# Optimization experiments

Measured on AMD Instinct MI355X. Metric: run time of the kernel, lower is better.

## Reference

```python
import jax, jax.numpy as jnp
import numpy as np

NUM_HEADS = 32
NUM_KV_HEADS = 8
HEAD_DIM = 128
ROPE_THETA = 10000.0


def rotate_half(x):
    x1, x2 = jnp.split(x, 2, axis=-1)
    return jnp.concatenate((-x2, x1), axis=-1)


def setup_inputs() -> dict:
    key = jax.random.key(0)
    ks = jax.random.split(key, 5)
    B, S, H = 1, 2048, 4096
    KV = NUM_KV_HEADS * HEAD_DIM
    return {
        "hidden_states": jax.random.normal(ks[0], (B, S, H), dtype=jnp.float32),
        "position_ids": jnp.arange(S, dtype=jnp.int64 if jax.config.jax_enable_x64 else jnp.int32)[None, :].repeat(B, axis=0),
        "Wq": jax.random.normal(ks[1], (H, H), dtype=jnp.float32) * 0.02,
        "Wk": jax.random.normal(ks[2], (KV, H), dtype=jnp.float32) * 0.02,
        "Wv": jax.random.normal(ks[3], (KV, H), dtype=jnp.float32) * 0.02,
        "Wo": jax.random.normal(ks[4], (H, H), dtype=jnp.float32) * 0.02,
    }


def reference(hidden_states, position_ids, Wq, Wk, Wv, Wo):
    B, S, H = hidden_states.shape
    nh, nkv, hd = NUM_HEADS, NUM_KV_HEADS, HEAD_DIM
    n_rep = nh // nkv

    # QKV projections (torch Linear: y = x @ W^T)
    q = jnp.einsum('bsh,oh->bso', hidden_states, Wq).reshape(B, S, nh, hd).transpose(0, 2, 1, 3)
    k = jnp.einsum('bsh,oh->bso', hidden_states, Wk).reshape(B, S, nkv, hd).transpose(0, 2, 1, 3)
    v = jnp.einsum('bsh,oh->bso', hidden_states, Wv).reshape(B, S, nkv, hd).transpose(0, 2, 1, 3)

    # RoPE: cos/sin [B, 1, S, hd]
    inv_freq = 1.0 / (ROPE_THETA ** (jnp.arange(0, hd, 2, dtype=jnp.float32) / hd))
    freqs = position_ids.astype(jnp.float32)[..., None] * inv_freq  # [B, S, hd/2]
    emb = jnp.concatenate((freqs, freqs), axis=-1)                  # [B, S, hd]
    cos = jnp.cos(emb)[:, None, :, :]
    sin = jnp.sin(emb)[:, None, :, :]
    q = q * cos + rotate_half(q) * sin
    k = k * cos + rotate_half(k) * sin

    # GQA repeat_kv: [B, nkv, S, hd] -> [B, nh, S, hd]
    k = jnp.repeat(k, n_rep, axis=1)
    v = jnp.repeat(v, n_rep, axis=1)

    # eager attention with causal mask, softmax in fp32
    scores = jnp.einsum('bhqd,bhkd->bhqk', q, k) / jnp.sqrt(jnp.float32(hd))
    causal = jnp.tril(jnp.ones((S, S), dtype=bool))
    scores = jnp.where(causal[None, None], scores, jnp.finfo(scores.dtype).min)
    probs = jax.nn.softmax(scores.astype(jnp.float32), axis=-1).astype(q.dtype)
    attn = jnp.einsum('bhqk,bhkd->bhqd', probs, v)

    out = attn.transpose(0, 2, 1, 3).reshape(B, S, nh * hd)
    return jnp.einsum('bso,ho->bsh', out, Wo)
```

## Files before the change

kernel.cpp:

```cpp
#include <hip/hip_runtime.h>

typedef __bf16 bf16x8 __attribute__((ext_vector_type(8)));
typedef float f32x4 __attribute__((ext_vector_type(4)));
typedef unsigned int u32x4 __attribute__((ext_vector_type(4)));
typedef unsigned short u16x4 __attribute__((ext_vector_type(4)));

#define S_LEN 2048
#define HDIM  4096
#define KVDIM 1024
#define NHEAD 32
#define NKV   8
#define QKVN  6144

__device__ __forceinline__ unsigned short f2b(float x) {
    unsigned int u = __builtin_bit_cast(unsigned int, x);
    u = (u + 0x7FFFu + ((u >> 16) & 1u)) >> 16;
    return (unsigned short)u;
}
__device__ __forceinline__ float b2f(unsigned short b) {
    unsigned int u = ((unsigned int)b) << 16;
    return __builtin_bit_cast(float, u);
}

__device__ __forceinline__ void gl_lds16(const void* g, void* s) {
    __builtin_amdgcn_global_load_lds(
        (const __attribute__((address_space(1))) unsigned int*)g,
        (__attribute__((address_space(3))) unsigned int*)s, 16, 0, 0);
}

__global__ void cvt_all(const float* __restrict__ hid, const float* __restrict__ Wq,
                        const float* __restrict__ Wk, const float* __restrict__ Wv,
                        unsigned short* __restrict__ hb, unsigned short* __restrict__ Wqkvb) {
    const int NH = S_LEN * HDIM / 4;
    const int NQ = HDIM * HDIM / 4;
    const int NK = KVDIM * HDIM / 4;
    int i = blockIdx.x * 256 + threadIdx.x;
    const float* src;
    unsigned short* dst;
    int off;
    if (i < NH) { src = hid; dst = hb; off = i; }
    else if (i < NH + NQ) { src = Wq; dst = Wqkvb; off = i - NH; }
    else if (i < NH + NQ + NK) { src = Wk; dst = Wqkvb + (size_t)HDIM * HDIM; off = i - NH - NQ; }
    else { src = Wv; dst = Wqkvb + (size_t)(HDIM + KVDIM) * HDIM; off = i - NH - NQ - NK; }
    f32x4 v = ((const f32x4*)src)[off];
    u16x4 o;
    o.x = f2b(v.x); o.y = f2b(v.y); o.z = f2b(v.z); o.w = f2b(v.w);
    ((u16x4*)dst)[off] = o;
}

__global__ void cvt_kernel(const float* __restrict__ in, unsigned short* __restrict__ out, int n4) {
    int i = blockIdx.x * 256 + threadIdx.x;
    if (i >= n4) return;
    f32x4 v = ((const f32x4*)in)[i];
    u16x4 o;
    o.x = f2b(v.x); o.y = f2b(v.y); o.z = f2b(v.z); o.w = f2b(v.w);
    ((u16x4*)out)[i] = o;
}

template <int MODE>
__device__ __forceinline__ void gemm_body(const unsigned short* __restrict__ A,
                                          const unsigned short* __restrict__ B,
                                          void* __restrict__ Cv,
                                          int M, int N, int K, int m0, int n0, int cn0,
                                          unsigned short (*As)[64], unsigned short (*Bs)[64]) {
    const int tid = threadIdx.x;
    const int w = tid >> 6, lane = tid & 63, quad = lane >> 4, l15 = lane & 15;
    const int wy = w >> 1, wx = w & 1;
    const int srowb = w * 32 + (lane >> 3);
    const int gchunk = (lane & 7) ^ (lane >> 3);
    const int lcol = (lane & 7) * 8;

    f32x4 acc[4][4] = {};

    for (int k0 = 0; k0 < K; k0 += 64) {
#pragma unroll
        for (int p = 0; p < 4; ++p) {
            int r = srowb + p * 8;
            gl_lds16(&A[(size_t)(m0 + r) * K + k0 + gchunk * 8], &As[r][lcol]);
            gl_lds16(&B[(size_t)(n0 + r) * K + k0 + gchunk * 8], &Bs[r][lcol]);
        }
        __syncthreads();
#pragma unroll
        for (int t = 0; t < 2; ++t) {
            bf16x8 af[4], bfr[4];
#pragma unroll
            for (int mb = 0; mb < 4; ++mb)
                af[mb] = *(const bf16x8*)&As[wy * 64 + mb * 16 + l15][(((t * 4 + quad) ^ (l15 & 7)) * 8)];
#pragma unroll
            for (int nb = 0; nb < 4; ++nb)
                bfr[nb] = *(const bf16x8*)&Bs[wx * 64 + nb * 16 + l15][(((t * 4 + quad) ^ (l15 & 7)) * 8)];
#pragma unroll
            for (int mb = 0; mb < 4; ++mb)
#pragma unroll
                for (int nb = 0; nb < 4; ++nb)
                    acc[mb][nb] = __builtin_amdgcn_mfma_f32_16x16x32_bf16(af[mb], bfr[nb], acc[mb][nb], 0, 0, 0);
        }
        __syncthreads();
    }
#pragma unroll
    for (int mb = 0; mb < 4; ++mb)
#pragma unroll
        for (int nb = 0; nb < 4; ++nb)
#pragma unroll
            for (int r = 0; r < 4; ++r) {
                int row = m0 + wy * 64 + mb * 16 + quad * 4 + r;
                int col = cn0 + wx * 64 + nb * 16 + l15;
                float v = acc[mb][nb][r];
                if (MODE == 0)
                    ((unsigned short*)Cv)[(size_t)row * N + col] = f2b(v);
                else if (MODE == 1)
                    ((unsigned short*)Cv)[(size_t)col * M + row] = f2b(v);
                else
                    ((float*)Cv)[(size_t)row * N + col] = v;
            }
}

template <int MODE>
__global__ __launch_bounds__(256) void gemm_nt(const unsigned short* __restrict__ A,
                                               const unsigned short* __restrict__ B,
                                               void* __restrict__ Cv, int M, int N, int K) {
    __shared__ unsigned short As[128][64];
    __shared__ unsigned short Bs[128][64];
    gemm_body<MODE>(A, B, Cv, M, N, K, blockIdx.y * 128, blockIdx.x * 128, blockIdx.x * 128, As, Bs);
}

__global__ __launch_bounds__(256) void gemm_qkv(const unsigned short* __restrict__ A,
                                                const unsigned short* __restrict__ W,
                                                unsigned short* __restrict__ Q,
                                                unsigned short* __restrict__ Kc,
                                                unsigned short* __restrict__ Vt,
                                                int M, int K) {
    __shared__ unsigned short As[128][64];
    __shared__ unsigned short Bs[128][64];
    const int bx = blockIdx.x, m0 = blockIdx.y * 128, n0 = bx * 128;
    if (bx < 32)
        gemm_body<0>(A, W, Q, M, HDIM, K, m0, n0, n0, As, Bs);
    else if (bx < 40)
        gemm_body<0>(A, W, Kc, M, KVDIM, K, m0, n0, n0 - HDIM, As, Bs);
    else
        gemm_body<1>(A, W, Vt, M, KVDIM, K, m0, n0, n0 - HDIM - KVDIM, As, Bs);
}

__global__ void rope_kernel(unsigned short* __restrict__ Q, unsigned short* __restrict__ Kc,
                            const int* __restrict__ pos_ids) {
    int tid = blockIdx.x * 256 + threadIdx.x;
    int j = tid & 63;
    int head = (tid >> 6) % (NHEAD + NKV);
    int s = tid / (64 * (NHEAD + NKV));
    float pos = (float)pos_ids[s];
    float inv = exp2f(-(float)j * 0.20762050593046f);
    float ang = pos * inv;
    float sn, cs;
    __sincosf(ang, &sn, &cs);
    unsigned short* p;
    if (head < NHEAD)
        p = Q + (size_t)s * HDIM + head * 128;
    else
        p = Kc + (size_t)s * KVDIM + (head - NHEAD) * 128;
    float x1 = b2f(p[j]), x2 = b2f(p[j + 64]);
    p[j] = f2b(x1 * cs - x2 * sn);
    p[j + 64] = f2b(x2 * cs + x1 * sn);
}

__global__ __launch_bounds__(256) void attn_fwd(const unsigned short* __restrict__ Q,
                                                const unsigned short* __restrict__ Kb,
                                                const unsigned short* __restrict__ Vt,
                                                unsigned short* __restrict__ O) {
    __shared__ unsigned short Ks[64][136];
    __shared__ unsigned short Vts[128][72];
    __shared__ unsigned short Ps[4][16][88];

    const int qblk = (gridDim.y - 1) - blockIdx.y;
    const int h = blockIdx.x, kvh = h >> 2;
    const int tid = threadIdx.x, w = tid >> 6, lane = tid & 63;
    const int quad = lane >> 4, l15 = lane & 15;
    const int qg = qblk * 64 + w * 16 + l15;

    bf16x8 aq[4];
#pragma unroll
    for (int t = 0; t < 4; ++t)
        aq[t] = *(const bf16x8*)&Q[(size_t)qg * HDIM + h * 128 + t * 32 + quad * 8];

    f32x4 o[8] = {};
    float m_s = -3.0e38f, l_s = 0.f;
    const float cexp = 0.08838834764831845f * 1.4426950408889634f;

    const int kr0 = tid >> 4, ksg = tid & 15;
    const int vr0 = tid >> 3, vsg = tid & 7;

    u32x4 kpre[4], vpre[4];
#pragma unroll
    for (int p = 0; p < 4; ++p) {
        kpre[p] = *(const u32x4*)&Kb[(size_t)(kr0 + p * 16) * KVDIM + kvh * 128 + ksg * 8];
        vpre[p] = *(const u32x4*)&Vt[(size_t)(kvh * 128 + vr0 + p * 32) * S_LEN + vsg * 8];
    }

    for (int kt = 0; kt <= qblk; ++kt) {
#pragma unroll
        for (int p = 0; p < 4; ++p) {
            *(u32x4*)&Ks[kr0 + p * 16][ksg * 8] = kpre[p];
            *(u32x4*)&Vts[vr0 + p * 32][vsg * 8] = vpre[p];
        }
        __syncthreads();
        if (kt < qblk) {
            const int k0n = kt * 64 + 64;
#pragma unroll
            for (int p = 0; p < 4; ++p) {
                kpre[p] = *(const u32x4*)&Kb[(size_t)(k0n + kr0 + p * 16) * KVDIM + kvh * 128 + ksg * 8];
                vpre[p] = *(const u32x4*)&Vt[(size_t)(kvh * 128 + vr0 + p * 32) * S_LEN + k0n + vsg * 8];
            }
        }

        f32x4 sc[4] = {};
        __builtin_amdgcn_s_setprio(1);
#pragma unroll
        for (int t = 0; t < 4; ++t)
#pragma unroll
            for (int mb = 0; mb < 4; ++mb) {
                bf16x8 ak = *(const bf16x8*)&Ks[mb * 16 + l15][t * 32 + quad * 8];
                sc[mb] = __builtin_amdgcn_mfma_f32_16x16x32_bf16(ak, aq[t], sc[mb], 0, 0, 0);
            }
        __builtin_amdgcn_s_setprio(0);

        float vv[16];
        if (kt == qblk) {
#pragma unroll
            for (int mb = 0; mb < 4; ++mb)
#pragma unroll
                for (int r = 0; r < 4; ++r) {
                    int kl = mb * 4 ? 0 : 0, _ = kl;
                    int kk = mb * 16 + quad * 4 + r;
                    vv[mb * 4 + r] = (kk <= w * 16 + l15) ? sc[mb][r] * cexp : -3.0e38f;
                }
        } else {
#pragma unroll
            for (int mb = 0; mb < 4; ++mb)
#pragma unroll
                for (int r = 0; r < 4; ++r)
                    vv[mb * 4 + r] = sc[mb][r] * cexp;
        }
        float m8[8];
#pragma unroll
        for (int i = 0; i < 8; ++i) m8[i] = fmaxf(vv[i], vv[i + 8]);
        float mx = fmaxf(fmaxf(fmaxf(m8[0], m8[1]), fmaxf(m8[2], m8[3])),
                         fmaxf(fmaxf(m8[4], m8[5]), fmaxf(m8[6], m8[7])));
        mx = fmaxf(mx, __shfl_xor(mx, 16, 64));
        mx = fmaxf(mx, __shfl_xor(mx, 32, 64));
        if (!__all(mx - m_s <= 8.0f)) {
            float mnew = fmaxf(m_s, mx);
            float alpha = exp2f(m_s - mnew);
            m_s = mnew;
            l_s *= alpha;
            float a4[4];
#pragma unroll
            for (int r = 0; r < 4; ++r) a4[r] = __shfl(alpha, quad * 20 + r, 64);
#pragma unroll
            for (int db = 0; db < 8; ++db)
#pragma unroll
                for (int r = 0; r < 4; ++r) o[db][r] *= a4[r];
        }
        float sum = 0.f;
        __bf16 pb[16] __attribute__((aligned(8)));
#pragma unroll
        for (int i = 0; i < 16; ++i) {
            float pp = exp2f(vv[i] - m_s);
            sum += pp;
            pb[i] = (__bf16)pp;
        }
        sum += __shfl_xor(sum, 16, 64);
        sum += __shfl_xor(sum, 32, 64);
        l_s += sum;
#pragma unroll
        for (int mb = 0; mb < 4; ++mb)
            *(u16x4*)&Ps[w][l15][mb * 16 + quad * 4] = *(const u16x4*)&pb[mb * 4];

        bf16x8 pa[2];
#pragma unroll
        for (int t = 0; t < 2; ++t)
            pa[t] = *(const bf16x8*)&Ps[w][l15][t * 32 + quad * 8];
        __builtin_amdgcn_s_setprio(1);
#pragma unroll
        for (int db = 0; db < 8; ++db)
#pragma unroll
            for (int t = 0; t < 2; ++t) {
                bf16x8 vb = *(const bf16x8*)&Vts[db * 16 + l15][t * 32 + quad * 8];
                o[db] = __builtin_amdgcn_mfma_f32_16x16x32_bf16(pa[t], vb, o[db], 0, 0, 0);
            }
        __builtin_amdgcn_s_setprio(0);
        __syncthreads();
    }

    float linv[4];
#pragma unroll
    for (int r = 0; r < 4; ++r) linv[r] = 1.0f / __shfl(l_s, quad * 20 + r, 64);
    const int qrow_base = qblk * 64 + w * 16 + quad * 4;
#pragma unroll
    for (int db = 0; db < 8; ++db)
#pragma unroll
        for (int r = 0; r < 4; ++r) {
            int row = qrow_base + r;
            int col = h * 128 + db * 16 + l15;
            O[(size_t)row * HDIM + col] = f2b(o[db][r] * linv[r]);
        }
}

extern "C" void kernel_launch(void* const* d_in, const int* in_sizes, int n_in,
                              void* d_out, int out_size, void* d_ws, size_t ws_size,
                              hipStream_t stream) {
    const float* hid = (const float*)d_in[0];
    const int* pos   = (const int*)d_in[1];
    const float* Wq  = (const float*)d_in[2];
    const float* Wk  = (const float*)d_in[3];
    const float* Wv  = (const float*)d_in[4];
    const float* Wo  = (const float*)d_in[5];
    float* out = (float*)d_out;

    char* ws = (char*)d_ws;
    unsigned short* hb    = (unsigned short*)(ws);
    unsigned short* Wqkvb = (unsigned short*)(ws + (16ull << 20));
    unsigned short* Wob   = (unsigned short*)(ws + (16ull << 20));
    unsigned short* Qw    = (unsigned short*)(ws + (64ull << 20));
    unsigned short* Kw    = (unsigned short*)(ws + (80ull << 20));
    unsigned short* Vtw   = (unsigned short*)(ws + (84ull << 20));
    unsigned short* attw  = hb;

    cvt_all<<<(S_LEN * HDIM / 4 + HDIM * HDIM / 4 + 2 * (KVDIM * HDIM / 4)) / 256, 256, 0, stream>>>(
        hid, Wq, Wk, Wv, hb, Wqkvb);

    gemm_qkv<<<dim3(QKVN / 128, S_LEN / 128), 256, 0, stream>>>(hb, Wqkvb, Qw, Kw, Vtw, S_LEN, HDIM);

    cvt_kernel<<<(HDIM * HDIM / 4 + 255) / 256, 256, 0, stream>>>(Wo, Wob, HDIM * HDIM / 4);

    rope_kernel<<<S_LEN * (NHEAD + NKV) * 64 / 256, 256, 0, stream>>>(Qw, Kw, pos);

    attn_fwd<<<dim3(NHEAD, S_LEN / 64), 256, 0, stream>>>(Qw, Kw, Vtw, attw);

    gemm_nt<2><<<dim3(HDIM / 128, S_LEN / 128), 256, 0, stream>>>(attw, Wob, out, S_LEN, HDIM, HDIM);
}
```

Baseline: 485.4 us.

## Merge Wo conversion with RoPE and use 128x256 tiles for output projection

The separate Wo fp32-to-bf16 conversion kernel and the RoPE kernel are combined into one launch, saving a kernel launch and its tail. The output projection GEMM moves to a 512-thread block with a 128x256 tile, so each A tile is reused across twice as many columns and the grid shrinks from 512 to 256 blocks. The larger tile raises LDS use per block and, with 256 blocks on a GPU with many CUs, may give less than one wave of blocks and uneven utilisation.

Result: no change. 493.9 us (+1.7%).

```diff
diff --git a/kernel.cpp b/kernel.cpp
--- a/kernel.cpp
+++ b/kernel.cpp
@@ -48,102 +48,19 @@
     ((u16x4*)dst)[off] = o;
 }
 
-__global__ void cvt_kernel(const float* __restrict__ in, unsigned short* __restrict__ out, int n4) {
-    int i = blockIdx.x * 256 + threadIdx.x;
-    if (i >= n4) return;
-    f32x4 v = ((const f32x4*)in)[i];
-    u16x4 o;
-    o.x = f2b(v.x); o.y = f2b(v.y); o.z = f2b(v.z); o.w = f2b(v.w);
-    ((u16x4*)out)[i] = o;
-}
-
-template <int MODE>
-__device__ __forceinline__ void gemm_body(const unsigned short* __restrict__ A,
-                                          const unsigned short* __restrict__ B,
-                                          void* __restrict__ Cv,
-                                          int M, int N, int K, int m0, int n0, int cn0,
-                                          unsigned short (*As)[64], unsigned short (*Bs)[64]) {
-    const int tid = threadIdx.x;
-    const int w = tid >> 6, lane = tid & 63, quad = lane >> 4, l15 = lane & 15;
-    const int wy = w >> 1, wx = w & 1;
-    const int srowb = w * 32 + (lane >> 3);
-    const int gchunk = (lane & 7) ^ (lane >> 3);
-    const int lcol = (lane & 7) * 8;
-
-    f32x4 acc[4][4] = {};
-
-    for (int k0 = 0; k0 < K; k0 += 64) {
-#pragma unroll
-        for (int p = 0; p < 4; ++p) {
-            int r = srowb + p * 8;
-            gl_lds16(&A[(size_t)(m0 + r) * K + k0 + gchunk * 8], &As[r][lcol]);
-            gl_lds16(&B[(size_t)(n0 + r) * K + k0 + gchunk * 8], &Bs[r][lcol]);
-        }
-        __syncthreads();
-#pragma unroll
-        for (int t = 0; t < 2; ++t) {
-            bf16x8 af[4], bfr[4];
-#pragma unroll
-            for (int mb = 0; mb < 4; ++mb)
-                af[mb] = *(const bf16x8*)&As[wy * 64 + mb * 16 + l15][(((t * 4 + quad) ^ (l15 & 7)) * 8)];
-#pragma unroll
-            for (int nb = 0; nb < 4; ++nb)
-                bfr[nb] = *(const bf16x8*)&Bs[wx * 64 + nb * 16 + l15][(((t * 4 + quad) ^ (l15 & 7)) * 8)];
-#pragma unroll
-            for (int mb = 0; mb < 4; ++mb)
-#pragma unroll
-                for (int nb = 0; nb < 4; ++nb)
-                    acc[mb][nb] = __builtin_amdgcn_mfma_f32_16x16x32_bf16(af[mb], bfr[nb], acc[mb][nb], 0, 0, 0);
-        }
-        __syncthreads();
-    }
-#pragma unroll
-    for (int mb = 0; mb < 4; ++mb)
-#pragma unroll
-        for (int nb = 0; nb < 4; ++nb)
-#pragma unroll
-            for (int r = 0; r < 4; ++r) {
-                int row = m0 + wy * 64 + mb * 16 + quad * 4 + r;
-                int col = cn0 + wx * 64 + nb * 16 + l15;
-                float v = acc[mb][nb][r];
-                if (MODE == 0)
-                    ((unsigned short*)Cv)[(size_t)row * N + col] = f2b(v);
-                else if (MODE == 1)
-                    ((unsigned short*)Cv)[(size_t)col * M + row] = f2b(v);
-                else
-                    ((float*)Cv)[(size_t)row * N + col] = v;
-            }
-}
-
-template <int MODE>
-__global__ __launch_bounds__(256) void gemm_nt(const unsigned short* __restrict__ A,
-                                               const unsigned short* __restrict__ B,
-                                               void* __restrict__ Cv, int M, int N, int K) {
-    __shared__ unsigned short As[128][64];
-    __shared__ unsigned short Bs[128][64];
-    gemm_body<MODE>(A, B, Cv, M, N, K, blockIdx.y * 128, blockIdx.x * 128, blockIdx.x * 128, As, Bs);
-}
-
-__global__ __launch_bounds__(256) void gemm_qkv(const unsigned short* __restrict__ A,
-                                                const unsigned short* __restrict__ W,
-                                                unsigned short* __restrict__ Q,
-                                                unsigned short* __restrict__ Kc,
-                                                unsigned short* __restrict__ Vt,
-                                                int M, int K) {
-    __shared__ unsigned short As[128][64];
-    __shared__ unsigned short Bs[128][64];
-    const int bx = blockIdx.x, m0 = blockIdx.y * 128, n0 = bx * 128;
-    if (bx < 32)
-        gemm_body<0>(A, W, Q, M, HDIM, K, m0, n0, n0, As, Bs);
-    else if (bx < 40)
-        gemm_body<0>(A, W, Kc, M, KVDIM, K, m0, n0, n0 - HDIM, As, Bs);
-    else
-        gemm_body<1>(A, W, Vt, M, KVDIM, K, m0, n0, n0 - HDIM - KVDIM, As, Bs);
-}
-
-__global__ void rope_kernel(unsigned short* __restrict__ Q, unsigned short* __restrict__ Kc,
+__global__ void post_kernel(const float* __restrict__ Wo, unsigned short* __restrict__ Wob,
+                            unsigned short* __restrict__ Q, unsigned short* __restrict__ Kc,
                             const int* __restrict__ pos_ids) {
-    int tid = blockIdx.x * 256 + threadIdx.x;
+    const int NWB = HDIM * HDIM / 4 / 256;
+    if (blockIdx.x < NWB) {
+        int i = blockIdx.x * 256 + threadIdx.x;
+        f32x4 v = ((const f32x4*)Wo)[i];
+        u16x4 o;
+        o.x = f2b(v.x); o.y = f2b(v.y); o.z = f2b(v.z); o.w = f2b(v.w);
+        ((u16x4*)Wob)[i] = o;
+        return;
+    }
+    int tid = (blockIdx.x - NWB) * 256 + threadIdx.x;
     int j = tid & 63;
     int head = (tid >> 6) % (NHEAD + NKV);
     int s = tid / (64 * (NHEAD + NKV));
@@ -162,6 +79,138 @@
     p[j + 64] = f2b(x2 * cs + x1 * sn);
 }
 
+template <int MODE>
+__device__ __forceinline__ void gemm_body(const unsigned short* __restrict__ A,
+                                          const unsigned short* __restrict__ B,
+                                          void* __restrict__ Cv,
+                                          int M, int N, int K, int m0, int n0, int cn0,
+                                          unsigned short (*As)[64], unsigned short (*Bs)[64]) {
+    const int tid = threadIdx.x;
+    const int w = tid >> 6, lane = tid & 63, quad = lane >> 4, l15 = lane & 15;
+    const int wy = w >> 1, wx = w & 1;
+    const int srowb = w * 32 + (lane >> 3);
+    const int gchunk = (lane & 7) ^ (lane >> 3);
+    const int lcol = (lane & 7) * 8;
+
+    f32x4 acc[4][4] = {};
+
+    for (int k0 = 0; k0 < K; k0 += 64) {
+#pragma unroll
+        for (int p = 0; p < 4; ++p) {
+            int r = srowb + p * 8;
+            gl_lds16(&A[(size_t)(m0 + r) * K + k0 + gchunk * 8], &As[r][lcol]);
+            gl_lds16(&B[(size_t)(n0 + r) * K + k0 + gchunk * 8], &Bs[r][lcol]);
+        }
+        __syncthreads();
+#pragma unroll
+        for (int t = 0; t < 2; ++t) {
+            bf16x8 af[4], bfr[4];
+#pragma unroll
+            for (int mb = 0; mb < 4; ++mb)
+                af[mb] = *(const bf16x8*)&As[wy * 64 + mb * 16 + l15][(((t * 4 + quad) ^ (l15 & 7)) * 8)];
+#pragma unroll
+            for (int nb = 0; nb < 4; ++nb)
+                bfr[nb] = *(const bf16x8*)&Bs[wx * 64 + nb * 16 + l15][(((t * 4 + quad) ^ (l15 & 7)) * 8)];
+#pragma unroll
+            for (int mb = 0; mb < 4; ++mb)
+#pragma unroll
+                for (int nb = 0; nb < 4; ++nb)
+                    acc[mb][nb] = __builtin_amdgcn_mfma_f32_16x16x32_bf16(af[mb], bfr[nb], acc[mb][nb], 0, 0, 0);
+        }
+        __syncthreads();
+    }
+#pragma unroll
+    for (int mb = 0; mb < 4; ++mb)
+#pragma unroll
+        for (int nb = 0; nb < 4; ++nb)
+#pragma unroll
+            for (int r = 0; r < 4; ++r) {
+                int row = m0 + wy * 64 + mb * 16 + quad * 4 + r;
+                int col = cn0 + wx * 64 + nb * 16 + l15;
+                float v = acc[mb][nb][r];
+                if (MODE == 0)
+                    ((unsigned short*)Cv)[(size_t)row * N + col] = f2b(v);
+                else if (MODE == 1)
+                    ((unsigned short*)Cv)[(size_t)col * M + row] = f2b(v);
+                else
+                    ((float*)Cv)[(size_t)row * N + col] = v;
+            }
+}
+
+__global__ __launch_bounds__(256) void gemm_qkv(const unsigned short* __restrict__ A,
+                                                const unsigned short* __restrict__ W,
+                                                unsigned short* __restrict__ Q,
+                                                unsigned short* __restrict__ Kc,
+                                                unsigned short* __restrict__ Vt,
+                                                int M, int K) {
+    __shared__ unsigned short As[128][64];
+    __shared__ unsigned short Bs[128][64];
+    const int bx = blockIdx.x, m0 = blockIdx.y * 128, n0 = bx * 128;
+    if (bx < 32)
+        gemm_body<0>(A, W, Q, M, HDIM, K, m0, n0, n0, As, Bs);
+    else if (bx < 40)
+        gemm_body<0>(A, W, Kc, M, KVDIM, K, m0, n0, n0 - HDIM, As, Bs);
+    else
+        gemm_body<1>(A, W, Vt, M, KVDIM, K, m0, n0, n0 - HDIM - KVDIM, As, Bs);
+}
+
+template <int MODE>
+__global__ __launch_bounds__(512) void gemm_wide(const unsigned short* __restrict__ A,
+                                                 const unsigned short* __restrict__ B,
+                                                 void* __restrict__ Cv, int M, int N, int K) {
+    __shared__ unsigned short As[128][64];
+    __shared__ unsigned short Bs[256][64];
+    const int tid = threadIdx.x;
+    const int w = tid >> 6, lane = tid & 63, quad = lane >> 4, l15 = lane & 15;
+    const int wy = w >> 2, wx = w & 3;
+    const int m0 = blockIdx.y * 128, n0 = blockIdx.x * 256;
+    const int srow = w * 8 + (lane >> 3);
+    const int gchunk = (lane & 7) ^ (lane >> 3);
+    const int lcol = (lane & 7) * 8;
+
+    f32x4 acc[4][4] = {};
+
+    for (int k0 = 0; k0 < K; k0 += 64) {
+#pragma unroll
+        for (int p = 0; p < 2; ++p)
+            gl_lds16(&A[(size_t)(m0 + p * 64 + srow) * K + k0 + gchunk * 8], &As[p * 64 + srow][lcol]);
+#pragma unroll
+        for (int p = 0; p < 4; ++p)
+            gl_lds16(&B[(size_t)(n0 + p * 64 + srow) * K + k0 + gchunk * 8], &Bs[p * 64 + srow][lcol]);
+        __syncthreads();
+#pragma unroll
+        for (int t = 0; t < 2; ++t) {
+            bf16x8 af[4], bfr[4];
+#pragma unroll
+            for (int mb = 0; mb < 4; ++mb)
+                af[mb] = *(const bf16x8*)&As[wy * 64 + mb * 16 + l15][(((t * 4 + quad) ^ (l15 & 7)) * 8)];
+#pragma unroll
+            for (int nb = 0; nb < 4; ++nb)
+                bfr[nb] = *(const bf16x8*)&Bs[wx * 64 + nb * 16 + l15][(((t * 4 + quad) ^ (l15 & 7)) * 8)];
+#pragma unroll
+            for (int mb = 0; mb < 4; ++mb)
+#pragma unroll
+                for (int nb = 0; nb < 4; ++nb)
+                    acc[mb][nb] = __builtin_amdgcn_mfma_f32_16x16x32_bf16(af[mb], bfr[nb], acc[mb][nb], 0, 0, 0);
+        }
+        __syncthreads();
+    }
+#pragma unroll
+    for (int mb = 0; mb < 4; ++mb)
+#pragma unroll
+        for (int nb = 0; nb < 4; ++nb)
+#pragma unroll
+            for (int r = 0; r < 4; ++r) {
+                int row = m0 + wy * 64 + mb * 16 + quad * 4 + r;
+                int col = n0 + wx * 64 + nb * 16 + l15;
+                float v = acc[mb][nb][r];
+                if (MODE == 0)
+                    ((unsigned short*)Cv)[(size_t)row * N + col] = f2b(v);
+                else if (MODE == 2)
+                    ((float*)Cv)[(size_t)row * N + col] = v;
+            }
+}
+
 __global__ __launch_bounds__(256) void attn_fwd(const unsigned short* __restrict__ Q,
                                                 const unsigned short* __restrict__ Kb,
                                                 const unsigned short* __restrict__ Vt,
@@ -228,7 +277,6 @@
             for (int mb = 0; mb < 4; ++mb)
 #pragma unroll
                 for (int r = 0; r < 4; ++r) {
-                    int kl = mb * 4 ? 0 : 0, _ = kl;
                     int kk = mb * 16 + quad * 4 + r;
                     vv[mb * 4 + r] = (kk <= w * 16 + l15) ? sc[mb][r] * cexp : -3.0e38f;
                 }
@@ -329,11 +377,10 @@
 
     gemm_qkv<<<dim3(QKVN / 128, S_LEN / 128), 256, 0, stream>>>(hb, Wqkvb, Qw, Kw, Vtw, S_LEN, HDIM);
 
-    cvt_kernel<<<(HDIM * HDIM / 4 + 255) / 256, 256, 0, stream>>>(Wo, Wob, HDIM * HDIM / 4);
-
-    rope_kernel<<<S_LEN * (NHEAD + NKV) * 64 / 256, 256, 0, stream>>>(Qw, Kw, pos);
+    post_kernel<<<HDIM * HDIM / 4 / 256 + S_LEN * (NHEAD + NKV) * 64 / 256, 256, 0, stream>>>(
+        Wo, Wob, Qw, Kw, pos);
 
     attn_fwd<<<dim3(NHEAD, S_LEN / 64), 256, 0, stream>>>(Qw, Kw, Vtw, attw);
 
-    gemm_nt<2><<<dim3(HDIM / 128, S_LEN / 128), 256, 0, stream>>>(attw, Wob, out, S_LEN, HDIM, HDIM);
-}
+    gemm_wide<2><<<dim3(HDIM / 256, S_LEN / 128), 512, 0, stream>>>(attw, Wob, out, S_LEN, HDIM, HDIM);
+}
```
